# Kernel tuning notes

Measured on AMD Instinct MI355X. Metric: run time of the kernel, lower is better.

Reference implementation:

```python
import jax, jax.numpy as jnp
import numpy as np

N = 20000   # nodes
E = 320000  # edges
D_IN = 256
D_OUT = 256


def setup_inputs() -> dict:
    key = jax.random.key(0)
    ks = jax.random.split(key, 12)
    s = 0.05
    return {
        "h": jax.random.normal(ks[0], (N, D_OUT), jnp.float32),
        "x": jax.random.normal(ks[1], (N, D_IN), jnp.float32),
        "pos": jax.random.normal(ks[2], (N, 3), jnp.float32),
        "W_fc": jax.random.normal(ks[3], (D_OUT, D_IN + D_OUT), jnp.float32) * s,
        "b_fc": jax.random.normal(ks[4], (D_OUT,), jnp.float32) * s,
        "W_conv": jax.random.normal(ks[5], (D_OUT, D_OUT), jnp.float32) * s,
        "W_ih": jax.random.normal(ks[6], (3 * D_OUT, D_OUT), jnp.float32) * s,
        "W_hh": jax.random.normal(ks[7], (3 * D_OUT, D_OUT), jnp.float32) * s,
        "b_ih": jax.random.normal(ks[8], (3 * D_OUT,), jnp.float32) * s,
        "b_hh": jax.random.normal(ks[9], (3 * D_OUT,), jnp.float32) * s,
        "edge_index_gate": jax.random.randint(ks[10], (2, E), 0, N, jnp.int64),
        "edge_index_cand": jax.random.randint(ks[11], (2, E), 0, N, jnp.int64),
    }


def reference(h, x, pos, W_fc, b_fc, W_conv, W_ih, W_hh, b_ih, b_hh,
              edge_index_gate, edge_index_cand):
    # fc + relu on concatenated [x, h]
    xh = jnp.concatenate([x, h], axis=-1)            # [N, in+out]
    xr = jax.nn.relu(xh @ W_fc.T + b_fc)             # [N, out]

    # GatedGraphConv, num_layers=1, aggr='add'
    m = xr @ W_conv                                  # [N, out]  (x @ weight[0])
    src, dst = edge_index_gate[0], edge_index_gate[1]
    agg = jax.ops.segment_sum(m[src], dst, num_segments=xr.shape[0])  # [N, out]

    # GRUCell(agg, xr)  (torch semantics: input=agg, hidden=xr)
    gi = agg @ W_ih.T + b_ih                         # [N, 3*out]
    gh = xr @ W_hh.T + b_hh                          # [N, 3*out]
    i_r, i_z, i_n = jnp.split(gi, 3, axis=-1)
    h_r, h_z, h_n = jnp.split(gh, 3, axis=-1)
    r = jax.nn.sigmoid(i_r + h_r)
    z = jax.nn.sigmoid(i_z + h_z)
    n = jnp.tanh(i_n + r * h_n)
    h_next = (1.0 - z) * n + z * xr
    return h_next
```

## Files before the change

kernel.cpp:

```cpp
#include <hip/hip_runtime.h>
#include <hip/hip_bf16.h>

#define N_NODES 20000
#define MPAD 20032
#define CAP 64

typedef __attribute__((ext_vector_type(8))) short short8;
typedef __attribute__((ext_vector_type(4))) float f32x4;

#define MFMA16(a,b,c) __builtin_amdgcn_mfma_f32_16x16x32_bf16(a,b,c,0,0,0)

#define FSW(r) (((r) & 3) ^ (((r) >> 2) & 3))

static __device__ __forceinline__ ushort f2bf(float f) {
  union { float f; uint u; } v; v.f = f;
  uint u = v.u;
  uint r = (u + 0x7FFFu + ((u >> 16) & 1u)) >> 16;
  return (ushort)r;
}
static __device__ __forceinline__ float bf2f(ushort s) {
  union { uint u; float f; } v; v.u = ((uint)s) << 16; return v.f;
}

typedef __attribute__((address_space(1))) const unsigned int guint;
typedef __attribute__((address_space(3))) unsigned int luint;
static __device__ __forceinline__ void gl2lds16(const void* g, void* l) {
  __builtin_amdgcn_global_load_lds((guint*)g, (luint*)l, 16, 0, 0);
}

static __device__ __forceinline__ void cvt8(const float* __restrict__ s, ushort* __restrict__ d) {
  float4 v0 = *(const float4*)s;
  float4 v1 = *(const float4*)(s + 4);
  union { ushort u[8]; uint4 v; } t;
  t.u[0]=f2bf(v0.x); t.u[1]=f2bf(v0.y); t.u[2]=f2bf(v0.z); t.u[3]=f2bf(v0.w);
  t.u[4]=f2bf(v1.x); t.u[5]=f2bf(v1.y); t.u[6]=f2bf(v1.z); t.u[7]=f2bf(v1.w);
  *(uint4*)d = t.v;
}

__global__ __launch_bounds__(256) void k_prep(
    const float* __restrict__ Wfc, const float* __restrict__ Wc,
    const float* __restrict__ Wih, const float* __restrict__ Whh,
    ushort* __restrict__ WfcB, ushort* __restrict__ WcB,
    ushort* __restrict__ WihB, ushort* __restrict__ Bg3, int* __restrict__ cnt) {
  int i = blockIdx.x * 256 + threadIdx.x;
  if (i < 16384) cvt8(Wfc + i * 8, WfcB + i * 8);
  if (i < 8192)  cvt8(Wc  + i * 8, WcB  + i * 8);
  if (i < 24576) cvt8(Wih + i * 8, WihB + i * 8);
  if (i < 24576) {
    int row = i >> 5;
    int k0 = (i & 31) * 8;
    int g = row / 48, rem = row - g * 48;
    int p = rem >> 4, ci = rem & 15;
    int c = g * 16 + ci;
    cvt8(Whh + ((size_t)(p * 256 + c)) * 256 + k0, Bg3 + (size_t)row * 512 + 256 + k0);
  }
  if (i < N_NODES) cnt[i] = 0;
}

__global__ __launch_bounds__(256, 3) void k_mid(
    const float* __restrict__ x, const float* __restrict__ h,
    const ushort* __restrict__ WfcB, const float* __restrict__ bfc,
    ushort* __restrict__ AX,
    const ushort* __restrict__ WihB, const ushort* __restrict__ WcB,
    ushort* __restrict__ Bg3,
    const int* __restrict__ eg, int* __restrict__ cnt, int* __restrict__ srcs) {
  __shared__ __attribute__((aligned(16))) ushort smem[64*32 + 128*32];
  int bid = blockIdx.x;
  int t = threadIdx.x, w = t >> 6, l = t & 63;

  if (bid >= 680) {
    int e = (bid - 680) * 256 + t;
    if (e < 320000) {
      int d = eg[320000 + e];
      int slot = atomicAdd(&cnt[d], 1);
      if (slot < CAP) srcs[d * CAP + slot] = eg[e];
    }
    return;
  }

  if (bid >= 632) {
    ushort* sA = smem;
    ushort* sB = smem + 64*32;
    int wf = bid - 632;
    int row0 = (wf % 12) * 64, col0 = (wf / 12) * 64;
    int wr = (w >> 1) * 32, wc = (w & 1) * 32;
    f32x4 acc[2][2] = {};
    for (int ks = 0; ks < 8; ++ks) {
      int k0 = ks * 32;
      {
        int r = t >> 2, wl = t & 3;
        int gw = wl ^ FSW(r);
        gl2lds16(WihB + (size_t)(row0 + r) * 256 + k0 + gw * 8,
                 (char*)sA + (size_t)(w * 64) * 16);
      }
      {
        int r = t >> 2, wl = t & 3;
        int gw = wl ^ FSW(r);
        gl2lds16(WcB + (size_t)(col0 + r) * 256 + k0 + gw * 8,
                 (char*)sB + (size_t)(w * 64) * 16);
      }
      __syncthreads();
      short8 af[2], bfr[2];
      #pragma unroll
      for (int mi = 0; mi < 2; ++mi) {
        int r = wr + mi * 16 + (l & 15);
        af[mi] = *(short8*)&sA[r * 32 + (((l >> 4)) ^ FSW(r)) * 8];
      }
      #pragma unroll
      for (int ni = 0; ni < 2; ++ni) {
        int br = wc + ni * 16 + (l & 15);
        bfr[ni] = *(short8*)&sB[br * 32 + (((l >> 4)) ^ FSW(br)) * 8];
      }
      #pragma unroll
      for (int mi = 0; mi < 2; ++mi)
        #pragma unroll
        for (int ni = 0; ni < 2; ++ni)
          acc[mi][ni] = MFMA16(af[mi], bfr[ni], acc[mi][ni]);
      __syncthreads();
    }
    #pragma unroll
    for (int mi = 0; mi < 2; ++mi)
      #pragma unroll
      for (int ni = 0; ni < 2; ++ni)
        #pragma unroll
        for (int q = 0; q < 4; ++q) {
          int jj = row0 + wr + mi*16 + (l>>4)*4 + q;
          int tc = col0 + wc + ni*16 + (l&15);
          int p = jj >> 8, c = jj & 255;
          int brow = (c >> 4) * 48 + p * 16 + (c & 15);
          Bg3[(size_t)brow * 512 + tc] = f2bf(acc[mi][ni][q]);
        }
    return;
  }

  ushort* sA = smem;
  ushort* sB = smem + 64*32;
  int wk = (bid & 7) * 79 + (bid >> 3);
  int panel = wk >> 1, ch = wk & 1;
  if (panel >= 313) return;
  int row0 = panel * 64, col0 = ch * 128;
  int wr = (w >> 1) * 32, wc = (w & 1) * 64;
  f32x4 acc[2][4] = {};
  for (int ks = 0; ks < 16; ++ks) {
    int k0 = ks * 32;
    const float* Af = (ks < 8) ? x : h;
    int ka = k0 & 255;
    {
      int r = t >> 2, wl = t & 3;
      int gw = wl ^ FSW(r);
      int gr = row0 + r; if (gr > N_NODES - 1) gr = N_NODES - 1;
      union { ushort u[8]; uint4 v; } tmp;
      const float* p = Af + (size_t)gr * 256 + ka + gw * 8;
      float4 v0 = *(const float4*)p;
      float4 v1 = *(const float4*)(p + 4);
      tmp.u[0]=f2bf(v0.x); tmp.u[1]=f2bf(v0.y); tmp.u[2]=f2bf(v0.z); tmp.u[3]=f2bf(v0.w);
      tmp.u[4]=f2bf(v1.x); tmp.u[5]=f2bf(v1.y); tmp.u[6]=f2bf(v1.z); tmp.u[7]=f2bf(v1.w);
      *(uint4*)&sA[r*32 + wl*8] = tmp.v;
    }
    #pragma unroll
    for (int j = 0; j < 2; ++j) {
      int ci = j * 256 + t;
      int br = ci >> 2, wl = ci & 3;
      int gw = wl ^ FSW(br);
      gl2lds16(WfcB + (size_t)(col0 + br) * 512 + k0 + gw * 8,
               (char*)sB + (size_t)(j * 256 + w * 64) * 16);
    }
    __syncthreads();
    short8 af[2], bfr[4];
    #pragma unroll
    for (int mi = 0; mi < 2; ++mi) {
      int r = wr + mi * 16 + (l & 15);
      af[mi] = *(short8*)&sA[r * 32 + (((l >> 4)) ^ FSW(r)) * 8];
    }
    #pragma unroll
    for (int ni = 0; ni < 4; ++ni) {
      int br = wc + ni * 16 + (l & 15);
      bfr[ni] = *(short8*)&sB[br * 32 + (((l >> 4)) ^ FSW(br)) * 8];
    }
    #pragma unroll
    for (int mi = 0; mi < 2; ++mi)
      #pragma unroll
      for (int ni = 0; ni < 4; ++ni)
        acc[mi][ni] = MFMA16(af[mi], bfr[ni], acc[mi][ni]);
    __syncthreads();
  }
  #pragma unroll
  for (int mi = 0; mi < 2; ++mi)
    #pragma unroll
    for (int ni = 0; ni < 4; ++ni)
      #pragma unroll
      for (int q = 0; q < 4; ++q) {
        int r = row0 + wr + mi*16 + (l>>4)*4 + q;
        int c = col0 + wc + ni*16 + (l&15);
        if (r < N_NODES) {
          float v = acc[mi][ni][q] + bfc[c];
          v = v > 0.f ? v : 0.f;
          AX[(size_t)r * 512 + 256 + c] = f2bf(v);
        }
      }
}

__global__ __launch_bounds__(256) void k_aggS(
    const int* __restrict__ cnt, const int* __restrict__ srcs,
    ushort* __restrict__ AX) {
  int node = blockIdx.x * 8 + (threadIdx.x >> 5);
  if (node >= N_NODES) return;
  int lane = threadIdx.x & 31;
  const int* bkt = srcs + node * CAP;
  int n = cnt[node]; if (n > CAP) n = CAP;
  float a[8] = {};
  int i = 0;
  for (; i + 4 <= n; i += 4) {
    uint4 v0 = *(const uint4*)(AX + (size_t)bkt[i  ] * 512 + 256 + lane * 8);
    uint4 v1 = *(const uint4*)(AX + (size_t)bkt[i+1] * 512 + 256 + lane * 8);
    uint4 v2 = *(const uint4*)(AX + (size_t)bkt[i+2] * 512 + 256 + lane * 8);
    uint4 v3 = *(const uint4*)(AX + (size_t)bkt[i+3] * 512 + 256 + lane * 8);
    const ushort* p0 = (const ushort*)&v0; const ushort* p1 = (const ushort*)&v1;
    const ushort* p2 = (const ushort*)&v2; const ushort* p3 = (const ushort*)&v3;
    #pragma unroll
    for (int j = 0; j < 8; j++) a[j] += (bf2f(p0[j]) + bf2f(p1[j])) + (bf2f(p2[j]) + bf2f(p3[j]));
  }
  for (; i < n; ++i) {
    uint4 v0 = *(const uint4*)(AX + (size_t)bkt[i] * 512 + 256 + lane * 8);
    const ushort* p0 = (const ushort*)&v0;
    #pragma unroll
    for (int j = 0; j < 8; j++) a[j] += bf2f(p0[j]);
  }
  union { ushort s[8]; uint4 v; } o;
  #pragma unroll
  for (int j = 0; j < 8; j++) o.s[j] = f2bf(a[j]);
  *(uint4*)(AX + (size_t)node * 512 + lane * 8) = o.v;
}

template<int PN>
static __device__ __forceinline__ void gru3_step(
    const ushort* __restrict__ AX, const ushort* __restrict__ Bg3,
    ushort* sA, ushort* sB, int row0, int bro, int w, int l, int ks,
    f32x4 (&acc)[4][4]) {
  int k0 = ks * 64;
  #pragma unroll
  for (int j = 0; j < 2; ++j) {
    int rb = w * 16 + j * 8;
    int r = rb + (l >> 3);
    int gw = (l & 7) ^ (r & 7);
    gl2lds16(AX + (size_t)(row0 + r) * 512 + k0 + gw * 8, (char*)sA + (size_t)rb * 128);
  }
  #pragma unroll
  for (int j = 0; j < 6; ++j) {
    int rb = j * 32 + w * 8;
    int r = rb + (l >> 3);
    int gw = (l & 7) ^ (r & 7);
    gl2lds16(Bg3 + (size_t)(bro + r) * 512 + k0 + gw * 8, (char*)sB + (size_t)rb * 128);
  }
  __syncthreads();
  #pragma unroll
  for (int j = 0; j < 2; ++j) {
    short8 af[4], bfr[3];
    #pragma unroll
    for (int mi = 0; mi < 4; ++mi) {
      int r = mi * 16 + (l & 15);
      af[mi] = *(short8*)&sA[r * 64 + ((j * 4 + (l >> 4)) ^ (r & 7)) * 8];
    }
    #pragma unroll
    for (int p = 0; p < 3; ++p) {
      int br = w * 48 + p * 16 + (l & 15);
      bfr[p] = *(short8*)&sB[br * 64 + ((j * 4 + (l >> 4)) ^ (br & 7)) * 8];
    }
    #pragma unroll
    for (int mi = 0; mi < 4; ++mi) {
      acc[mi][0]  = MFMA16(af[mi], bfr[0], acc[mi][0]);
      acc[mi][1]  = MFMA16(af[mi], bfr[1], acc[mi][1]);
      acc[mi][PN] = MFMA16(af[mi], bfr[2], acc[mi][PN]);
    }
  }
  __syncthreads();
}

__global__ __launch_bounds__(256, 4) void k_gru3(
    const ushort* __restrict__ AX, const ushort* __restrict__ Bg3,
    const float* __restrict__ bih, const float* __restrict__ bhh,
    float* __restrict__ out) {
  __shared__ __attribute__((aligned(16))) ushort sA[64*64];
  __shared__ __attribute__((aligned(16))) ushort sB[192*64];
  int bid = blockIdx.x;
  int wk = (bid & 7) * 157 + (bid >> 3);
  int panel = wk >> 2, ch = wk & 3;
  if (panel >= 313) return;
  int row0 = panel * 64;
  int bro = ch * 192;
  int t = threadIdx.x, w = t >> 6, l = t & 63;
  f32x4 acc[4][4] = {};
  for (int ks = 0; ks < 4; ++ks)
    gru3_step<2>(AX, Bg3, sA, sB, row0, bro, w, l, ks, acc);
  for (int ks = 4; ks < 8; ++ks)
    gru3_step<3>(AX, Bg3, sA, sB, row0, bro, w, l, ks, acc);

  int c = ch * 64 + w * 16 + (l & 15);
  float br_ = bih[c] + bhh[c];
  float bz_ = bih[256 + c] + bhh[256 + c];
  float bi_ = bih[512 + c];
  float bh_ = bhh[512 + c];
  #pragma unroll
  for (int mi = 0; mi < 4; ++mi)
    #pragma unroll
    for (int q = 0; q < 4; ++q) {
      int r = row0 + mi*16 + (l>>4)*4 + q;
      if (r < N_NODES) {
        float rg = 1.f / (1.f + __expf(-(acc[mi][0][q] + br_)));
        float zg = 1.f / (1.f + __expf(-(acc[mi][1][q] + bz_)));
        float ng = tanhf((acc[mi][2][q] + bi_) + rg * (acc[mi][3][q] + bh_));
        float xv = bf2f(AX[(size_t)r * 512 + 256 + c]);
        out[(size_t)r * 256 + c] = (1.f - zg) * ng + zg * xv;
      }
    }
}

extern "C" void kernel_launch(void* const* d_in, const int* in_sizes, int n_in,
                              void* d_out, int out_size, void* d_ws, size_t ws_size,
                              hipStream_t stream) {
  const float* h   = (const float*)d_in[0];
  const float* x   = (const float*)d_in[1];
  const float* Wfc = (const float*)d_in[3];
  const float* bfc = (const float*)d_in[4];
  const float* Wc  = (const float*)d_in[5];
  const float* Wih = (const float*)d_in[6];
  const float* Whh = (const float*)d_in[7];
  const float* bih = (const float*)d_in[8];
  const float* bhh = (const float*)d_in[9];
  const int*   eg  = (const int*)d_in[10];
  float* out = (float*)d_out;

  char* ws = (char*)d_ws;
  ushort* AX   = (ushort*)(ws);
  ushort* WfcB = (ushort*)(ws + 20512768);
  ushort* WcB  = (ushort*)(ws + 20774912);
  ushort* WihB = (ushort*)(ws + 20905984);
  ushort* Bg3  = (ushort*)(ws + 21299200);
  int*    cnt    = (int*)(ws + 22085632);
  int*    srcs   = (int*)(ws + 22165632);

  k_prep<<<512, 256, 0, stream>>>(Wfc, Wc, Wih, Whh, WfcB, WcB, WihB, Bg3, cnt);

  k_mid<<<1930, 256, 0, stream>>>(x, h, WfcB, bfc, AX, WihB, WcB, Bg3, eg, cnt, srcs);

  k_aggS<<<(N_NODES + 7) / 8, 256, 0, stream>>>(cnt, srcs, AX);

  k_gru3<<<1256, 256, 0, stream>>>(AX, Bg3, bih, bhh, out);
}
```

Baseline: 97.50 us.

## Double-buffer LDS tiles in fc GEMM and GRU GEMM to overlap loads with MFMA

```diff
diff --git a/kernel.cpp b/kernel.cpp
--- a/kernel.cpp
+++ b/kernel.cpp
@@ -57,6 +57,35 @@
   if (i < N_NODES) cnt[i] = 0;
 }
 
+static __device__ __forceinline__ void fc_loadA(
+    const float* __restrict__ x, const float* __restrict__ h,
+    int gr, int gw, int ks, float4& v0, float4& v1) {
+  const float* Af = (ks < 8) ? x : h;
+  int ka = (ks * 32) & 255;
+  const float* p = Af + (size_t)gr * 256 + ka + gw * 8;
+  v0 = *(const float4*)p;
+  v1 = *(const float4*)(p + 4);
+}
+static __device__ __forceinline__ void fc_writeA(ushort* sA, int r, int wl,
+                                                 float4 v0, float4 v1) {
+  union { ushort u[8]; uint4 v; } tmp;
+  tmp.u[0]=f2bf(v0.x); tmp.u[1]=f2bf(v0.y); tmp.u[2]=f2bf(v0.z); tmp.u[3]=f2bf(v0.w);
+  tmp.u[4]=f2bf(v1.x); tmp.u[5]=f2bf(v1.y); tmp.u[6]=f2bf(v1.z); tmp.u[7]=f2bf(v1.w);
+  *(uint4*)&sA[r*32 + wl*8] = tmp.v;
+}
+static __device__ __forceinline__ void fc_stageB(
+    const ushort* __restrict__ WfcB, ushort* sB, int col0, int t, int w, int ks) {
+  int k0 = ks * 32;
+  #pragma unroll
+  for (int j = 0; j < 2; ++j) {
+    int ci = j * 256 + t;
+    int br = ci >> 2, wl = ci & 3;
+    int gw = wl ^ FSW(br);
+    gl2lds16(WfcB + (size_t)(col0 + br) * 512 + k0 + gw * 8,
+             (char*)sB + (size_t)(j * 256 + w * 64) * 16);
+  }
+}
+
 __global__ __launch_bounds__(256, 3) void k_mid(
     const float* __restrict__ x, const float* __restrict__ h,
     const ushort* __restrict__ WfcB, const float* __restrict__ bfc,
@@ -64,7 +93,7 @@
     const ushort* __restrict__ WihB, const ushort* __restrict__ WcB,
     ushort* __restrict__ Bg3,
     const int* __restrict__ eg, int* __restrict__ cnt, int* __restrict__ srcs) {
-  __shared__ __attribute__((aligned(16))) ushort smem[64*32 + 128*32];
+  __shared__ __attribute__((aligned(16))) ushort smem[12288];
   int bid = blockIdx.x;
   int t = threadIdx.x, w = t >> 6, l = t & 63;
 
@@ -80,7 +109,7 @@
 
   if (bid >= 632) {
     ushort* sA = smem;
-    ushort* sB = smem + 64*32;
+    ushort* sB = smem + 2048;
     int wf = bid - 632;
     int row0 = (wf % 12) * 64, col0 = (wf / 12) * 64;
     int wr = (w >> 1) * 32, wc = (w & 1) * 32;
@@ -133,49 +162,48 @@
     return;
   }
 
-  ushort* sA = smem;
-  ushort* sB = smem + 64*32;
+  ushort* sA0 = smem;
+  ushort* sA1 = smem + 2048;
+  ushort* sB0 = smem + 4096;
+  ushort* sB1 = smem + 8192;
   int wk = (bid & 7) * 79 + (bid >> 3);
   int panel = wk >> 1, ch = wk & 1;
   if (panel >= 313) return;
   int row0 = panel * 64, col0 = ch * 128;
   int wr = (w >> 1) * 32, wc = (w & 1) * 64;
+  int r_ = t >> 2, wl_ = t & 3;
+  int gw_ = wl_ ^ FSW(r_);
+  int gr_ = row0 + r_; if (gr_ > N_NODES - 1) gr_ = N_NODES - 1;
+
+  float4 va0, va1;
+  fc_loadA(x, h, gr_, gw_, 0, va0, va1);
+  fc_writeA(sA0, r_, wl_, va0, va1);
+  fc_stageB(WfcB, sB0, col0, t, w, 0);
+  fc_loadA(x, h, gr_, gw_, 1, va0, va1);
+  __syncthreads();
+
   f32x4 acc[2][4] = {};
+  #pragma unroll
   for (int ks = 0; ks < 16; ++ks) {
-    int k0 = ks * 32;
-    const float* Af = (ks < 8) ? x : h;
-    int ka = k0 & 255;
-    {
-      int r = t >> 2, wl = t & 3;
-      int gw = wl ^ FSW(r);
-      int gr = row0 + r; if (gr > N_NODES - 1) gr = N_NODES - 1;
-      union { ushort u[8]; uint4 v; } tmp;
-      const float* p = Af + (size_t)gr * 256 + ka + gw * 8;
-      float4 v0 = *(const float4*)p;
-      float4 v1 = *(const float4*)(p + 4);
-      tmp.u[0]=f2bf(v0.x); tmp.u[1]=f2bf(v0.y); tmp.u[2]=f2bf(v0.z); tmp.u[3]=f2bf(v0.w);
-      tmp.u[4]=f2bf(v1.x); tmp.u[5]=f2bf(v1.y); tmp.u[6]=f2bf(v1.z); tmp.u[7]=f2bf(v1.w);
-      *(uint4*)&sA[r*32 + wl*8] = tmp.v;
-    }
-    #pragma unroll
-    for (int j = 0; j < 2; ++j) {
-      int ci = j * 256 + t;
-      int br = ci >> 2, wl = ci & 3;
-      int gw = wl ^ FSW(br);
-      gl2lds16(WfcB + (size_t)(col0 + br) * 512 + k0 + gw * 8,
-               (char*)sB + (size_t)(j * 256 + w * 64) * 16);
-    }
-    __syncthreads();
+    ushort* cA = (ks & 1) ? sA1 : sA0;
+    ushort* cB = (ks & 1) ? sB1 : sB0;
+    ushort* nA = (ks & 1) ? sA0 : sA1;
+    ushort* nB = (ks & 1) ? sB0 : sB1;
+    if (ks < 15) {
+      fc_writeA(nA, r_, wl_, va0, va1);
+      fc_stageB(WfcB, nB, col0, t, w, ks + 1);
+      if (ks < 14) fc_loadA(x, h, gr_, gw_, ks + 2, va0, va1);
+    }
     short8 af[2], bfr[4];
     #pragma unroll
     for (int mi = 0; mi < 2; ++mi) {
       int r = wr + mi * 16 + (l & 15);
-      af[mi] = *(short8*)&sA[r * 32 + (((l >> 4)) ^ FSW(r)) * 8];
+      af[mi] = *(short8*)&cA[r * 32 + (((l >> 4)) ^ FSW(r)) * 8];
     }
     #pragma unroll
     for (int ni = 0; ni < 4; ++ni) {
       int br = wc + ni * 16 + (l & 15);
-      bfr[ni] = *(short8*)&sB[br * 32 + (((l >> 4)) ^ FSW(br)) * 8];
+      bfr[ni] = *(short8*)&cB[br * 32 + (((l >> 4)) ^ FSW(br)) * 8];
     }
     #pragma unroll
     for (int mi = 0; mi < 2; ++mi)
@@ -232,11 +260,9 @@
   *(uint4*)(AX + (size_t)node * 512 + lane * 8) = o.v;
 }
 
-template<int PN>
-static __device__ __forceinline__ void gru3_step(
+static __device__ __forceinline__ void gru3_stage(
     const ushort* __restrict__ AX, const ushort* __restrict__ Bg3,
-    ushort* sA, ushort* sB, int row0, int bro, int w, int l, int ks,
-    f32x4 (&acc)[4][4]) {
+    ushort* sA, ushort* sB, int row0, int bro, int w, int l, int ks) {
   int k0 = ks * 64;
   #pragma unroll
   for (int j = 0; j < 2; ++j) {
@@ -252,19 +278,23 @@
     int gw = (l & 7) ^ (r & 7);
     gl2lds16(Bg3 + (size_t)(bro + r) * 512 + k0 + gw * 8, (char*)sB + (size_t)rb * 128);
   }
-  __syncthreads();
+}
+
+template<int PN>
+static __device__ __forceinline__ void gru3_compute(
+    const ushort* sA, const ushort* sB, int w, int l, f32x4 (&acc)[4][4]) {
   #pragma unroll
   for (int j = 0; j < 2; ++j) {
     short8 af[4], bfr[3];
     #pragma unroll
     for (int mi = 0; mi < 4; ++mi) {
       int r = mi * 16 + (l & 15);
-      af[mi] = *(short8*)&sA[r * 64 + ((j * 4 + (l >> 4)) ^ (r & 7)) * 8];
+      af[mi] = *(const short8*)&sA[r * 64 + ((j * 4 + (l >> 4)) ^ (r & 7)) * 8];
     }
     #pragma unroll
     for (int p = 0; p < 3; ++p) {
       int br = w * 48 + p * 16 + (l & 15);
-      bfr[p] = *(short8*)&sB[br * 64 + ((j * 4 + (l >> 4)) ^ (br & 7)) * 8];
+      bfr[p] = *(const short8*)&sB[br * 64 + ((j * 4 + (l >> 4)) ^ (br & 7)) * 8];
     }
     #pragma unroll
     for (int mi = 0; mi < 4; ++mi) {
@@ -273,15 +303,17 @@
       acc[mi][PN] = MFMA16(af[mi], bfr[2], acc[mi][PN]);
     }
   }
-  __syncthreads();
-}
-
-__global__ __launch_bounds__(256, 4) void k_gru3(
+}
+
+__global__ __launch_bounds__(256, 2) void k_gru3(
     const ushort* __restrict__ AX, const ushort* __restrict__ Bg3,
     const float* __restrict__ bih, const float* __restrict__ bhh,
     float* __restrict__ out) {
-  __shared__ __attribute__((aligned(16))) ushort sA[64*64];
-  __shared__ __attribute__((aligned(16))) ushort sB[192*64];
+  __shared__ __attribute__((aligned(16))) ushort smem[2 * 16384];
+  ushort* sA0 = smem;
+  ushort* sB0 = smem + 4096;
+  ushort* sA1 = smem + 16384;
+  ushort* sB1 = smem + 20480;
   int bid = blockIdx.x;
   int wk = (bid & 7) * 157 + (bid >> 3);
   int panel = wk >> 2, ch = wk & 3;
@@ -289,11 +321,22 @@
   int row0 = panel * 64;
   int bro = ch * 192;
   int t = threadIdx.x, w = t >> 6, l = t & 63;
+
+  gru3_stage(AX, Bg3, sA0, sB0, row0, bro, w, l, 0);
+  __syncthreads();
+
   f32x4 acc[4][4] = {};
-  for (int ks = 0; ks < 4; ++ks)
-    gru3_step<2>(AX, Bg3, sA, sB, row0, bro, w, l, ks, acc);
-  for (int ks = 4; ks < 8; ++ks)
-    gru3_step<3>(AX, Bg3, sA, sB, row0, bro, w, l, ks, acc);
+  #pragma unroll
+  for (int ks = 0; ks < 8; ++ks) {
+    ushort* cA = (ks & 1) ? sA1 : sA0;
+    ushort* cB = (ks & 1) ? sB1 : sB0;
+    ushort* nA = (ks & 1) ? sA0 : sA1;
+    ushort* nB = (ks & 1) ? sB0 : sB1;
+    if (ks < 7) gru3_stage(AX, Bg3, nA, nB, row0, bro, w, l, ks + 1);
+    if (ks < 4) gru3_compute<2>(cA, cB, w, l, acc);
+    else        gru3_compute<3>(cA, cB, w, l, acc);
+    __syncthreads();
+  }
 
   int c = ch * 64 + w * 16 + (l & 15);
   float br_ = bih[c] + bhh[c];
```

New measurement: 100.0 us. 2.6% more time.
